# Kernel optimization log

Hardware: AMD Instinct MI355X
Metric: run time of the kernel (lower is better)

Reference implementation:

```python
import jax, jax.numpy as jnp
import numpy as np
import math

B, S, D, NH = 2, 2048, 1024, 16
DK = D // NH
E, TOPK, MOE_H, NSH = 8, 2, 1024, 2
SH_H = MOE_H * NSH
EPS = 1e-6


def setup_inputs() -> dict:
    key = jax.random.key(0)
    ks = jax.random.split(key, 24)
    p = lambda k, shape: jax.random.normal(k, shape, jnp.float32) * 0.02
    x = jax.random.normal(ks[0], (B, S, D), jnp.float32)
    # RoPE tables: freqs_cis = exp(i * t * theta^{-2j/dk}), passed as cos/sin
    inv = 1.0 / (10000.0 ** (np.arange(0, DK, 2, dtype=np.float32) / DK))
    ang = np.outer(np.arange(S, dtype=np.float32), inv)
    freqs_cos = jnp.asarray(np.cos(ang), jnp.float32)
    freqs_sin = jnp.asarray(np.sin(ang), jnp.float32)
    mask = jnp.triu(jnp.full((S, S), -1e9, jnp.float32), k=1)  # causal additive mask
    return {
        'x': x, 'freqs_cos': freqs_cos, 'freqs_sin': freqs_sin, 'mask': mask,
        'wq': p(ks[1], (D, D)), 'wk': p(ks[2], (D, D)),
        'wv': p(ks[3], (D, D)), 'wo': p(ks[4], (D, D)),
        'attn_norm_w': jnp.ones((D,), jnp.float32),
        'ffn_norm_w': jnp.ones((D,), jnp.float32),
        'gate_w': p(ks[5], (E, D)), 'gate_b': p(ks[6], (E,)),
        'w1': p(ks[7], (E, MOE_H, D)), 'b1': p(ks[8], (E, MOE_H)),
        'w2': p(ks[9], (E, D, MOE_H)), 'b2': p(ks[10], (E, D)),
        'w3': p(ks[11], (E, MOE_H, D)), 'b3': p(ks[12], (E, MOE_H)),
        'sg_w': p(ks[13], (SH_H, D)), 'su_w': p(ks[14], (SH_H, D)),
        'sd_w': p(ks[15], (D, SH_H)),
    }


def rmsnorm(x, w):
    f = x.astype(jnp.float32)
    y = f * jax.lax.rsqrt(jnp.mean(f * f, axis=-1, keepdims=True) + EPS)
    return y.astype(x.dtype) * w


def rope(t, cos, sin):
    # t: [b, s, h, dk]; pairs (t[2j], t[2j+1]) as complex, multiplied by e^{i ang}
    tr, ti = t[..., 0::2], t[..., 1::2]
    c, s = cos[None, :, None, :], sin[None, :, None, :]
    outr = tr * c - ti * s
    outi = tr * s + ti * c
    return jnp.stack([outr, outi], axis=-1).reshape(t.shape)


def reference(x, freqs_cos, freqs_sin, mask, wq, wk, wv, wo, attn_norm_w, ffn_norm_w,
              gate_w, gate_b, w1, b1, w2, b2, w3, b3, sg_w, su_w, sd_w):
    b, s, d = x.shape
    # --- attention with RoPE ---
    h = rmsnorm(x, attn_norm_w)
    q = (h @ wq.T).reshape(b, s, NH, DK)
    k = (h @ wk.T).reshape(b, s, NH, DK)
    v = (h @ wv.T).reshape(b, s, NH, DK)
    q = rope(q, freqs_cos, freqs_sin)
    k = rope(k, freqs_cos, freqs_sin)
    scale = 1.0 / math.sqrt(DK)
    q = q.transpose(0, 2, 1, 3)
    k = k.transpose(0, 2, 1, 3)
    v = v.transpose(0, 2, 1, 3)
    scores = jnp.einsum('bhqd,bhkd->bhqk', q, k) * scale + mask
    # NOTE: source divides by sqrt(d_k) a second time before softmax (faithful quirk)
    attn = jax.nn.softmax(scores * scale, axis=-1)
    o = jnp.einsum('bhqk,bhkd->bhqd', attn, v).transpose(0, 2, 1, 3).reshape(b, s, d)
    x = x + o @ wo.T
    # --- MoE FFN ---
    hf = rmsnorm(x, ffn_norm_w).reshape(-1, d)                 # [T, D]
    gscores = jax.nn.softmax(hf @ gate_w.T + gate_b, axis=-1)  # [T, E]
    _, idx = jax.lax.top_k(gscores, TOPK)                      # bias is None -> topk on scores
    weights = jnp.take_along_axis(gscores, idx, axis=1)        # original_scores gather
    wmask = (jax.nn.one_hot(idx, E, dtype=hf.dtype) * weights[..., None]).sum(1)  # [T, E]
    shared = (jax.nn.silu(hf @ sg_w.T) * (hf @ su_w.T)) @ sd_w.T
    a1 = jnp.einsum('td,ehd->teh', hf, w1) + b1
    a3 = jnp.einsum('td,ehd->teh', hf, w3) + b3
    eo = jnp.einsum('teh,edh->ted', jax.nn.silu(a1) * a3, w2) + b2  # [T, E, D]
    router = jnp.einsum('te,ted->td', wmask, eo)
    return x + (shared + router).reshape(x.shape)
```

## Files before the change

### kernel.cpp

```cpp
#include <hip/hip_runtime.h>


typedef unsigned short u16;
typedef __attribute__((ext_vector_type(8))) short bh8;
typedef __attribute__((ext_vector_type(4))) float fv4;
typedef __attribute__((ext_vector_type(4))) unsigned uv4;
typedef __attribute__((ext_vector_type(2))) int iv2;

#define LOG2E 1.4426950408889634f
#define MAX_TILES 71

__device__ __forceinline__ float b2f(u16 u) {
  return __builtin_bit_cast(float, ((unsigned)u) << 16);
}
__device__ __forceinline__ u16 f2b(float f) {
  unsigned x = __builtin_bit_cast(unsigned, f);
  return (u16)((x + 0x7fffu + ((x >> 16) & 1u)) >> 16);
}
__device__ __forceinline__ fv4 mfma16(bh8 a, bh8 b, fv4 c) {
  return __builtin_amdgcn_mfma_f32_16x16x32_bf16(a, b, c, 0, 0, 0);
}
__device__ __forceinline__ unsigned cvtpk(float lo, float hi) {
  unsigned r;
  asm("v_cvt_pk_bf16_f32 %0, %1, %2" : "=v"(r) : "v"(lo), "v"(hi));
  return r;
}

#define GLD16(g, l)                                                        \
  __builtin_amdgcn_global_load_lds(                                        \
      (const __attribute__((address_space(1))) void*)(g),                  \
      (__attribute__((address_space(3))) void*)(l), 16, 0, 0)

__device__ __forceinline__ bh8 lds_frag(const u16* base, int row, int b8) {
  int off = row * 128 + ((b8 * 16) ^ ((row & 7) << 4));
  return *(const bh8*)((const char*)base + off);
}

template <int MODE, int TM = 128>
__global__ __launch_bounds__(256) void gemm_bt(
    const u16* __restrict__ A, const u16* __restrict__ B, int M, int N, int K,
    u16* __restrict__ Cb, float* __restrict__ Cf,
    const float* __restrict__ add1, const float* __restrict__ add2,
    const float* __restrict__ bias, const int* __restrict__ tmeta,
    const int* __restrict__ etok) {
  constexpr int MR = TM / 32;
  __shared__ u16 As[TM * 64];
  __shared__ u16 Bs[128 * 64];
  const int lane = threadIdx.x & 63;
  const int wid = threadIdx.x >> 6;
  const int wr = wid >> 1, wc = wid & 1;
  const int n0 = blockIdx.x * 128;
  const int rr = lane >> 3;
  const int b8s = (lane & 7) ^ rr;
  const int ldA = (MODE == 6) ? M : K;

  int m0 = 0, e = 0, m0l = 0, cnt = 0, row0 = 0;
  const u16* Bp = B;
  if constexpr (MODE == 6 || MODE == 8) {
    int tile = blockIdx.y;
    if (tile >= tmeta[0]) return;
    e = tmeta[16 + tile * 4];
    m0l = tmeta[17 + tile * 4];
    cnt = tmeta[18 + tile * 4];
    row0 = tmeta[19 + tile * 4];
    Bp = B + (size_t)e * N * K;
  } else {
    m0 = blockIdx.y * TM;
  }

  const u16* Arow[MR];
  const u16* Brow[4];
#pragma unroll
  for (int i = 0; i < MR; ++i) {
    int c = wid * MR + i;
    int row = c * 8 + rr;
    if constexpr (MODE == 8) {
      int li = m0l + row;
      li = li < cnt ? li : cnt - 1;
      int tok = etok[e * 4096 + li];
      Arow[i] = A + (size_t)tok * ldA + b8s * 8;
    } else if constexpr (MODE == 6) {
      Arow[i] = A + (size_t)(row0 + row) * ldA + b8s * 8;
    } else {
      Arow[i] = A + (size_t)(m0 + row) * ldA + b8s * 8;
    }
  }
#pragma unroll
  for (int i = 0; i < 4; ++i)
    Brow[i] = Bp + (size_t)(n0 + (wid * 4 + i) * 8 + rr) * K + b8s * 8;

  fv4 acc[MR][4] = {};
  for (int k0 = 0; k0 < K; k0 += 64) {
    __syncthreads();
#pragma unroll
    for (int i = 0; i < MR; ++i)
      GLD16(Arow[i] + k0, &As[(wid * MR + i) * 512]);
#pragma unroll
    for (int i = 0; i < 4; ++i)
      GLD16(Brow[i] + k0, &Bs[(wid * 4 + i) * 512]);
    __syncthreads();
#pragma unroll
    for (int ks = 0; ks < 2; ++ks) {
      int b8 = ks * 4 + (lane >> 4);
      bh8 af[MR], bf[4];
#pragma unroll
      for (int mi = 0; mi < MR; ++mi)
        af[mi] = lds_frag(As, wr * (16 * MR) + mi * 16 + (lane & 15), b8);
#pragma unroll
      for (int ni = 0; ni < 4; ++ni)
        bf[ni] = lds_frag(Bs, wc * 64 + ni * 16 + (lane & 15), b8);
      __builtin_amdgcn_s_setprio(1);
#pragma unroll
      for (int mi = 0; mi < MR; ++mi)
#pragma unroll
        for (int ni = 0; ni < 4; ++ni)
          acc[mi][ni] = mfma16(af[mi], bf[ni], acc[mi][ni]);
      __builtin_amdgcn_s_setprio(0);
    }
  }

  const int rbase = (MODE == 6 || MODE == 8) ? row0 : m0;
  const int r0b = rbase + wr * (16 * MR) + (lane >> 4) * 4;

  if constexpr (MODE == 7 || MODE == 8) {
    const int OUTN = N >> 1;
    const int colb = (n0 >> 1) + wc * 32;
    const float* bb1 = nullptr;
    const float* bb3 = nullptr;
    if constexpr (MODE == 8) {
      bb1 = add1 + (size_t)e * OUTN;
      bb3 = add2 + (size_t)e * OUTN;
    }
#pragma unroll
    for (int mi = 0; mi < MR; ++mi) {
#pragma unroll
      for (int ni = 0; ni < 2; ++ni) {
        int c = colb + ni * 16 + (lane & 15);
#pragma unroll
        for (int r = 0; r < 4; ++r) {
          int row = r0b + mi * 16 + r;
          float xg = acc[mi][ni][r];
          float yu = acc[mi][ni + 2][r];
          if constexpr (MODE == 8) {
            xg += bb1[c];
            yu += bb3[c];
          }
          float s = xg / (1.f + __expf(-xg));
          Cb[(size_t)row * OUTN + c] = f2b(s * yu);
        }
      }
    }
  } else {
    const int c0b = n0 + wc * 64 + (lane & 15);
    const float* bb = nullptr;
    if constexpr (MODE == 6) bb = bias + (size_t)e * N;
#pragma unroll
    for (int mi = 0; mi < MR; ++mi) {
#pragma unroll
      for (int ni = 0; ni < 4; ++ni) {
        int c = c0b + ni * 16;
#pragma unroll
        for (int r = 0; r < 4; ++r) {
          int row = r0b + mi * 16 + r;
          size_t idx = (size_t)row * N + c;
          float v = acc[mi][ni][r];
          if constexpr (MODE == 0) Cb[idx] = f2b(v);
          else if constexpr (MODE == 1) Cf[idx] = add1[idx] + v;
          else if constexpr (MODE == 4) Cf[idx] = add1[idx] + add2[idx] + v;
          else Cb[idx] = f2b(v + bb[c]);
        }
      }
    }
  }
}

__global__ __launch_bounds__(256) void rmsnorm_bf16(
    const float* __restrict__ x, const float* __restrict__ w,
    u16* __restrict__ out) {
  int t = blockIdx.x;
  const float* xr = x + (size_t)t * 1024;
  fv4 v = *(const fv4*)(xr + threadIdx.x * 4);
  float ss = v[0] * v[0] + v[1] * v[1] + v[2] * v[2] + v[3] * v[3];
#pragma unroll
  for (int off = 1; off < 64; off <<= 1) ss += __shfl_xor(ss, off);
  __shared__ float red[4];
  int lane = threadIdx.x & 63, wid = threadIdx.x >> 6;
  if (lane == 0) red[wid] = ss;
  __syncthreads();
  float inv = rsqrtf((red[0] + red[1] + red[2] + red[3]) * (1.0f / 1024.f) + 1e-6f);
  u16* op = out + (size_t)t * 1024 + threadIdx.x * 4;
  const float* wp = w + threadIdx.x * 4;
#pragma unroll
  for (int i = 0; i < 4; ++i) op[i] = f2b(v[i] * inv * wp[i]);
}

__global__ __launch_bounds__(256) void rope_repack(
    const u16* __restrict__ qkv, const float* __restrict__ fc,
    const float* __restrict__ fs, u16* __restrict__ qr, u16* __restrict__ kr,
    u16* __restrict__ vt, int S) {
  __shared__ u16 tile[64][65];
  const int s0 = blockIdx.x * 64;
  const int b = blockIdx.y;
  const int h0 = blockIdx.z * 4;
#pragma unroll 4
  for (int it = 0; it < 32; ++it) {
    int idx = threadIdx.x + it * 256;
    int tl = idx >> 7, rem = idx & 127;
    int h = h0 + (rem >> 5), i = rem & 31;
    int s = s0 + tl;
    float c = fc[s * 32 + i], sn = fs[s * 32 + i];
    size_t src = ((size_t)(b * S + s)) * 3072 + h * 64 + 2 * i;
    size_t dst = ((size_t)((b * 16 + h) * S + s)) * 64 + 2 * i;
    float a0 = b2f(qkv[src]), a1 = b2f(qkv[src + 1]);
    qr[dst] = f2b(a0 * c - a1 * sn);
    qr[dst + 1] = f2b(a0 * sn + a1 * c);
    float b0 = b2f(qkv[src + 1024]), b1 = b2f(qkv[src + 1025]);
    kr[dst] = f2b(b0 * c - b1 * sn);
    kr[dst + 1] = f2b(b0 * sn + b1 * c);
  }
  for (int hh = 0; hh < 4; ++hh) {
    int h = h0 + hh;
    __syncthreads();
    for (int cc = threadIdx.x; cc < 512; cc += 256) {
      int tl = cc >> 3, d8 = cc & 7;
      bh8 val = *(const bh8*)(qkv + ((size_t)(b * S + s0 + tl)) * 3072 + 2048 +
                              h * 64 + d8 * 8);
#pragma unroll
      for (int j = 0; j < 8; ++j) tile[tl][d8 * 8 + j] = (u16)val[j];
    }
    __syncthreads();
    for (int cc = threadIdx.x; cc < 512; cc += 256) {
      int d = cc >> 3, pg = cc & 7;
      int sbase = 16 * (pg >> 2) + 4 * (pg & 3);
      bh8 o;
#pragma unroll
      for (int j = 0; j < 8; ++j)
        o[j] = (short)tile[sbase + (j & 3) + ((j >> 2) << 5)][d];
      *(bh8*)(vt + ((size_t)((b * 16 + h) * 64 + d)) * S + s0 + pg * 8) = o;
    }
  }
}

__global__ __launch_bounds__(256) void attn_fwd(
    const u16* __restrict__ qr, const u16* __restrict__ kr,
    const u16* __restrict__ vt, u16* __restrict__ ob, int S, int NHc) {
  __shared__ u16 Ks[2][64 * 64];
  __shared__ u16 Vs[2][64 * 64];
  const int lane = threadIdx.x & 63;
  const int wid = threadIdx.x >> 6;
  const int g = lane >> 4;
  const int l15 = lane & 15;
  const int bh = blockIdx.x;
  const int ia = blockIdx.y;
  const int nq = S / 64;
  const int qa0 = ia * 64;
  const int qb0 = (nq - 1 - ia) * 64;
  const int b = bh / NHc, h = bh % NHc;
  const u16* qbase = qr + (size_t)bh * S * 64;
  const u16* kb = kr + (size_t)bh * S * 64;
  const u16* vb = vt + (size_t)bh * 64 * S;
  const float SC = 0.015625f * LOG2E;
  const int rr = lane >> 3;
  const int b8s = (lane & 7) ^ rr;

  bh8 ONES;
#pragma unroll
  for (int j = 0; j < 8; ++j) ONES[j] = (short)0x3f80;

  bh8 qfA[2], qfB[2];
  {
    const u16* qp = qbase + (size_t)(qa0 + wid * 16 + l15) * 64 + g * 8;
    qfA[0] = *(const bh8*)qp;
    qfA[1] = *(const bh8*)(qp + 32);
    qp = qbase + (size_t)(qb0 + wid * 16 + l15) * 64 + g * 8;
    qfB[0] = *(const bh8*)qp;
    qfB[1] = *(const bh8*)(qp + 32);
  }
  fv4 oaccA[4] = {}, oaccB[4] = {};
  fv4 lA = {}, lB = {};
  float mA = -1e30f, mB = -1e30f;
  const int nktB = nq - ia;

  auto stage = [&](int buf, int j0) {
#pragma unroll
    for (int i = 0; i < 2; ++i) {
      int c = wid * 2 + i;
      int row = c * 8 + rr;
      GLD16(kb + (size_t)(j0 + row) * 64 + b8s * 8, &Ks[buf][c * 512]);
      GLD16(vb + (size_t)row * S + j0 + b8s * 8, &Vs[buf][c * 512]);
    }
  };
  stage(0, 0);

  auto process = [&](const bh8 (&kf)[2][4], const bh8 (&vf)[2][4], int j0,
                     int q0x, bh8* qf, fv4* oacc, float& mrow, fv4& lrowC) {
    const int q_my = q0x + wid * 16 + l15;
    fv4 st[4] = {};
    __builtin_amdgcn_s_setprio(1);
#pragma unroll
    for (int ks = 0; ks < 2; ++ks)
#pragma unroll
      for (int jt = 0; jt < 4; ++jt)
        st[jt] = mfma16(kf[ks][jt], qf[ks], st[jt]);
    __builtin_amdgcn_s_setprio(0);

    float sr[4][4];
    float mloc = -1e30f;
    const int jb = j0 + 4 * g;
    if (j0 + 63 > q0x + wid * 16) {
#pragma unroll
      for (int jt = 0; jt < 4; ++jt)
#pragma unroll
        for (int r = 0; r < 4; ++r) {
          int j = jb + jt * 16 + r;
          float s = (j <= q_my) ? st[jt][r] : -1e30f;
          sr[jt][r] = s;
          mloc = fmaxf(mloc, s);
        }
    } else {
#pragma unroll
      for (int jt = 0; jt < 4; ++jt)
#pragma unroll
        for (int r = 0; r < 4; ++r) {
          sr[jt][r] = st[jt][r];
          mloc = fmaxf(mloc, st[jt][r]);
        }
    }
    mloc = fmaxf(mloc, __shfl_xor(mloc, 16));
    mloc = fmaxf(mloc, __shfl_xor(mloc, 32));
    mloc *= SC;
    bool defer = __all(mloc <= mrow + 8.f);
    if (!defer) {
      float mnew = fmaxf(mrow, mloc);
      float sfac = exp2f(mrow - mnew);
      mrow = mnew;
      float sfC[4];
#pragma unroll
      for (int r = 0; r < 4; ++r) sfC[r] = __shfl(sfac, g * 4 + r);
#pragma unroll
      for (int dt = 0; dt < 4; ++dt)
#pragma unroll
        for (int r = 0; r < 4; ++r) oacc[dt][r] *= sfC[r];
#pragma unroll
      for (int r = 0; r < 4; ++r) lrowC[r] *= sfC[r];
    }
    float p[4][4];
#pragma unroll
    for (int jt = 0; jt < 4; ++jt)
#pragma unroll
      for (int r = 0; r < 4; ++r)
        p[jt][r] = exp2f(fmaf(sr[jt][r], SC, -mrow));

    __builtin_amdgcn_s_setprio(1);
    fv4 racc = {};
#pragma unroll
    for (int ks = 0; ks < 2; ++ks) {
      uv4 w;
      w[0] = cvtpk(p[ks][0], p[ks][1]);
      w[1] = cvtpk(p[ks][2], p[ks][3]);
      w[2] = cvtpk(p[ks + 2][0], p[ks + 2][1]);
      w[3] = cvtpk(p[ks + 2][2], p[ks + 2][3]);
      bh8 pa = __builtin_bit_cast(bh8, w);
      racc = mfma16(pa, ONES, racc);
#pragma unroll
      for (int dt = 0; dt < 4; ++dt)
        oacc[dt] = mfma16(pa, vf[ks][dt], oacc[dt]);
    }
    __builtin_amdgcn_s_setprio(0);
#pragma unroll
    for (int r = 0; r < 4; ++r) lrowC[r] += racc[r];
  };

  for (int kt = 0; kt < nktB; ++kt) {
    const int j0 = kt * 64;
    __syncthreads();
    if (kt + 1 < nktB) stage((kt + 1) & 1, (kt + 1) * 64);
    const u16* Kc = Ks[kt & 1];
    const u16* Vc = Vs[kt & 1];
    bh8 kf[2][4], vf[2][4];
#pragma unroll
    for (int ks = 0; ks < 2; ++ks) {
      int b8 = ks * 4 + g;
#pragma unroll
      for (int jt = 0; jt < 4; ++jt)
        kf[ks][jt] = lds_frag(Kc, jt * 16 + l15, b8);
#pragma unroll
      for (int dt = 0; dt < 4; ++dt)
        vf[ks][dt] = lds_frag(Vc, dt * 16 + l15, b8);
    }
    process(kf, vf, j0, qb0, qfB, oaccB, mB, lB);
    if (kt <= ia) process(kf, vf, j0, qa0, qfA, oaccA, mA, lA);
  }

  auto wout = [&](fv4* oacc, fv4 lrowC, int q0x) {
#pragma unroll
    for (int dt = 0; dt < 4; ++dt)
#pragma unroll
      for (int r = 0; r < 4; ++r) {
        int row = q0x + wid * 16 + g * 4 + r;
        int col = dt * 16 + l15;
        ob[((size_t)b * S + row) * 1024 + h * 64 + col] =
            f2b(oacc[dt][r] / lrowC[r]);
      }
  };
  wout(oaccA, lA, qa0);
  wout(oaccB, lB, qb0);
}

__global__ __launch_bounds__(256) void gate_topk(
    const float* __restrict__ x2, const float* __restrict__ nw,
    const float* __restrict__ gw, const float* __restrict__ gb,
    int* __restrict__ topk_e, float* __restrict__ topk_w) {
  int t = blockIdx.x * 4 + (threadIdx.x >> 6);
  int lane = threadIdx.x & 63;
  const float* xr = x2 + (size_t)t * 1024;
  float hv[16];
  float ss = 0.f;
#pragma unroll
  for (int i = 0; i < 4; ++i) {
    fv4 v = *(const fv4*)(xr + lane * 16 + i * 4);
#pragma unroll
    for (int j = 0; j < 4; ++j) {
      hv[i * 4 + j] = v[j];
      ss += v[j] * v[j];
    }
  }
#pragma unroll
  for (int off = 1; off < 64; off <<= 1) ss += __shfl_xor(ss, off);
  float inv = rsqrtf(ss * (1.0f / 1024.f) + 1e-6f);
  const fv4* nwp = (const fv4*)(nw + lane * 16);
#pragma unroll
  for (int i = 0; i < 4; ++i) {
    fv4 wv = nwp[i];
#pragma unroll
    for (int j = 0; j < 4; ++j) hv[i * 4 + j] *= inv * wv[j];
  }
  float logit[8];
#pragma unroll
  for (int e = 0; e < 8; ++e) {
    const fv4* wp = (const fv4*)(gw + (size_t)e * 1024 + lane * 16);
    float s = 0.f;
#pragma unroll
    for (int i = 0; i < 4; ++i) {
      fv4 wv = wp[i];
#pragma unroll
      for (int j = 0; j < 4; ++j) s += hv[i * 4 + j] * wv[j];
    }
    logit[e] = s;
  }
#pragma unroll
  for (int off = 1; off < 64; off <<= 1)
#pragma unroll
    for (int e = 0; e < 8; ++e) logit[e] += __shfl_xor(logit[e], off);
  if (lane == 0) {
#pragma unroll
    for (int e = 0; e < 8; ++e) logit[e] += gb[e];
    float mx = logit[0];
#pragma unroll
    for (int e = 1; e < 8; ++e) mx = fmaxf(mx, logit[e]);
    float pe[8], se = 0.f;
#pragma unroll
    for (int e = 0; e < 8; ++e) { pe[e] = __expf(logit[e] - mx); se += pe[e]; }
    float rs = 1.f / se;
#pragma unroll
    for (int e = 0; e < 8; ++e) pe[e] *= rs;
    int i0 = 0;
    float b0 = pe[0];
#pragma unroll
    for (int e = 1; e < 8; ++e)
      if (pe[e] > b0) { b0 = pe[e]; i0 = e; }
    int i1 = -1;
    float b1v = -1.f;
#pragma unroll
    for (int e = 0; e < 8; ++e)
      if (e != i0 && pe[e] > b1v) { b1v = pe[e]; i1 = e; }
    topk_e[2 * t] = i0;
    topk_e[2 * t + 1] = i1;
    topk_w[2 * t] = b0;
    topk_w[2 * t + 1] = b1v;
  }
}

__global__ __launch_bounds__(512) void route_tokens(
    const int* __restrict__ topk_e, int* __restrict__ pos_of,
    int* __restrict__ etok, int* __restrict__ meta, int T2) {
  __shared__ int scnt[8];
  const int e = threadIdx.x >> 6;
  const int lane = threadIdx.x & 63;
  int base = 0;
  for (int i0 = 0; i0 < T2; i0 += 128) {
    iv2 te = *(const iv2*)(topk_e + i0 + lane * 2);
    unsigned long long m0 = __ballot(te[0] == e);
    unsigned long long m1 = __ballot(te[1] == e);
    unsigned long long lt = (1ull << lane) - 1;
    int pre = __popcll(m0 & lt) + __popcll(m1 & lt);
    if (te[0] == e) {
      int pos = base + pre;
      etok[e * 4096 + pos] = (i0 >> 1) + lane;
      pos_of[i0 + lane * 2] = pos;
      ++pre;
    }
    if (te[1] == e) {
      int pos = base + pre;
      etok[e * 4096 + pos] = (i0 >> 1) + lane;
      pos_of[i0 + lane * 2 + 1] = pos;
    }
    base += __popcll(m0) + __popcll(m1);
  }
  if (lane == 0) scnt[e] = base;
  __syncthreads();
  if (threadIdx.x == 0) {
    int tt = 0, rb = 0;
#pragma unroll
    for (int e2 = 0; e2 < 8; ++e2) {
      meta[1 + e2] = rb;
      int c = scnt[e2];
      int nt = (c + 127) >> 7;
      for (int i = 0; i < nt; ++i) {
        meta[16 + tt * 4] = e2;
        meta[17 + tt * 4] = i * 128;
        meta[18 + tt * 4] = c;
        meta[19 + tt * 4] = rb + i * 128;
        ++tt;
      }
      rb += nt * 128;
    }
    meta[0] = tt;
  }
}

__global__ __launch_bounds__(128) void combine_router(
    const u16* __restrict__ eo, const int* __restrict__ topk_e,
    const float* __restrict__ topk_w, const int* __restrict__ pos_of,
    const int* __restrict__ meta, float* __restrict__ router) {
  int t = blockIdx.x;
  int c = threadIdx.x * 8;
  int e0 = topk_e[2 * t], e1 = topk_e[2 * t + 1];
  float w0 = topk_w[2 * t], w1 = topk_w[2 * t + 1];
  int r0 = meta[1 + e0] + pos_of[2 * t];
  int r1 = meta[1 + e1] + pos_of[2 * t + 1];
  bh8 v0 = *(const bh8*)(eo + (size_t)r0 * 1024 + c);
  bh8 v1 = *(const bh8*)(eo + (size_t)r1 * 1024 + c);
  float* rp = router + (size_t)t * 1024 + c;
#pragma unroll
  for (int j = 0; j < 8; ++j)
    rp[j] = w0 * b2f((u16)v0[j]) + w1 * b2f((u16)v1[j]);
}

__global__ __launch_bounds__(256) void f2b_convert(
    const float* __restrict__ src, u16* __restrict__ dst) {
  size_t i = ((size_t)blockIdx.x * 256 + threadIdx.x) * 8;
  fv4 a = *(const fv4*)(src + i);
  fv4 b = *(const fv4*)(src + i + 4);
  bh8 o;
#pragma unroll
  for (int j = 0; j < 4; ++j) o[j] = (short)f2b(a[j]);
#pragma unroll
  for (int j = 0; j < 4; ++j) o[4 + j] = (short)f2b(b[j]);
  *(bh8*)(dst + i) = o;
}

__global__ __launch_bounds__(256) void f2b_convert_ilv(
    const float* __restrict__ src, u16* __restrict__ dst, int half,
    int seg_shift) {
  size_t i = ((size_t)blockIdx.x * 256 + threadIdx.x) * 8;
  int r = (int)(i >> 10), col = (int)(i & 1023);
  int rl = r & ((1 << seg_shift) - 1), e = r >> seg_shift;
  int dstrow = (e << (seg_shift + 1)) + ((rl >> 5) << 6) + (rl & 31) +
               (half << 5);
  fv4 a = *(const fv4*)(src + i);
  fv4 b = *(const fv4*)(src + i + 4);
  bh8 o;
#pragma unroll
  for (int j = 0; j < 4; ++j) o[j] = (short)f2b(a[j]);
#pragma unroll
  for (int j = 0; j < 4; ++j) o[4 + j] = (short)f2b(b[j]);
  *(bh8*)(dst + (size_t)dstrow * 1024 + col) = o;
}

extern "C" void kernel_launch(void* const* d_in, const int* in_sizes, int n_in,
                              void* d_out, int out_size, void* d_ws,
                              size_t ws_size, hipStream_t stream) {
  (void)in_sizes; (void)n_in; (void)out_size; (void)ws_size;
  const int Sc = 2048, Dc = 1024, NHc = 16, Tc = 4096, SH = 2048;

  const float* x   = (const float*)d_in[0];
  const float* fc  = (const float*)d_in[1];
  const float* fs  = (const float*)d_in[2];
  const float* wq  = (const float*)d_in[4];
  const float* wk  = (const float*)d_in[5];
  const float* wv  = (const float*)d_in[6];
  const float* wo  = (const float*)d_in[7];
  const float* anw = (const float*)d_in[8];
  const float* fnw = (const float*)d_in[9];
  const float* gw  = (const float*)d_in[10];
  const float* gb  = (const float*)d_in[11];
  const float* w1  = (const float*)d_in[12];
  const float* b1  = (const float*)d_in[13];
  const float* w2  = (const float*)d_in[14];
  const float* b2  = (const float*)d_in[15];
  const float* w3  = (const float*)d_in[16];
  const float* b3  = (const float*)d_in[17];
  const float* sgw = (const float*)d_in[18];
  const float* suw = (const float*)d_in[19];
  const float* sdw = (const float*)d_in[20];
  float* out = (float*)d_out;

  char* base = (char*)d_ws;
  size_t off = 0;
  auto alloc = [&](size_t bytes) -> void* {
    void* p = base + off;
    off += (bytes + 255) & ~(size_t)255;
    return p;
  };
  u16* wqkv_b = (u16*)alloc(2ull * 3072 * 1024);
  u16* wo_b   = (u16*)alloc(2ull * 1024 * 1024);
  u16* sgu_b  = (u16*)alloc(2ull * 4096 * 1024);
  u16* sdw_b  = (u16*)alloc(2ull * 1024 * 2048);
  u16* w13_b  = (u16*)alloc(2ull * 8 * 2048 * 1024);
  u16* w2_b   = (u16*)alloc(2ull * 8 * 1024 * 1024);
  char* regA = (char*)alloc(2ull * Tc * 4096);
  char* regB = (char*)alloc(2ull * (size_t)MAX_TILES * 128 * 2048);
  float* x2  = (float*)alloc(4ull * Tc * Dc);
  u16* hs_b  = (u16*)alloc(2ull * Tc * SH);
  int* topk_e = (int*)alloc(2ull * Tc * 4);
  float* topk_w = (float*)alloc(2ull * Tc * 4);
  int* pos_of = (int*)alloc(2ull * Tc * 4);
  int* etok = (int*)alloc(8ull * 4096 * 4);
  int* meta = (int*)alloc(512 * 4);

  u16* qkv_out = (u16*)regA;
  u16* eo_c    = (u16*)regA;
  u16* h_b  = (u16*)regB;
  u16* qr   = (u16*)regB;
  u16* kr   = (u16*)(regB + 2ull * Tc * Dc);
  u16* vt_  = (u16*)(regB + 4ull * Tc * Dc);
  u16* o_b  = (u16*)(regB + 6ull * Tc * Dc);
  u16* a13_c = (u16*)regB;
  float* router = (float*)regB;
  u16* hf_b = wqkv_b;

  auto conv = [&](const float* s, u16* d, size_t n) {
    f2b_convert<<<dim3((unsigned)(n / 2048)), 256, 0, stream>>>(s, d);
  };
  conv(wq, wqkv_b, (size_t)Dc * Dc);
  conv(wk, wqkv_b + 1048576, (size_t)Dc * Dc);
  conv(wv, wqkv_b + 2097152, (size_t)Dc * Dc);
  conv(wo, wo_b, (size_t)Dc * Dc);
  conv(sdw, sdw_b, (size_t)Dc * SH);
  conv(w2, w2_b, 8ull * 1024 * 1024);
  f2b_convert_ilv<<<1024, 256, 0, stream>>>(sgw, sgu_b, 0, 11);
  f2b_convert_ilv<<<1024, 256, 0, stream>>>(suw, sgu_b, 1, 11);
  f2b_convert_ilv<<<4096, 256, 0, stream>>>(w1, w13_b, 0, 10);
  f2b_convert_ilv<<<4096, 256, 0, stream>>>(w3, w13_b, 1, 10);

  rmsnorm_bf16<<<Tc, 256, 0, stream>>>(x, anw, h_b);
  gemm_bt<0><<<dim3(3072 / 128, Tc / 128), 256, 0, stream>>>(
      h_b, wqkv_b, Tc, 3072, Dc, qkv_out, nullptr, nullptr, nullptr, nullptr,
      nullptr, nullptr);
  rope_repack<<<dim3(Sc / 64, 2, 4), 256, 0, stream>>>(qkv_out, fc, fs, qr, kr,
                                                       vt_, Sc);
  attn_fwd<<<dim3(2 * NHc, Sc / 128), 256, 0, stream>>>(qr, kr, vt_, o_b, Sc,
                                                        NHc);
  gemm_bt<1, 64><<<dim3(Dc / 128, Tc / 64), 256, 0, stream>>>(
      o_b, wo_b, Tc, Dc, Dc, nullptr, x2, x, nullptr, nullptr, nullptr,
      nullptr);

  rmsnorm_bf16<<<Tc, 256, 0, stream>>>(x2, fnw, hf_b);
  gate_topk<<<Tc / 4, 256, 0, stream>>>(x2, fnw, gw, gb, topk_e, topk_w);
  route_tokens<<<1, 512, 0, stream>>>(topk_e, pos_of, etok, meta, 2 * Tc);

  gemm_bt<7><<<dim3(4096 / 128, Tc / 128), 256, 0, stream>>>(
      hf_b, sgu_b, Tc, 4096, Dc, hs_b, nullptr, nullptr, nullptr, nullptr,
      nullptr, nullptr);

  gemm_bt<8><<<dim3(2048 / 128, MAX_TILES), 256, 0, stream>>>(
      hf_b, w13_b, Tc, 2048, Dc, a13_c, nullptr, b1, b3, nullptr, meta, etok);
  gemm_bt<6><<<dim3(Dc / 128, MAX_TILES), 256, 0, stream>>>(
      a13_c, w2_b, 1024, Dc, 1024, eo_c, nullptr, nullptr, nullptr,
      b2, meta, etok);
  combine_router<<<Tc, 128, 0, stream>>>(eo_c, topk_e, topk_w, pos_of, meta,
                                         router);

  gemm_bt<4, 64><<<dim3(Dc / 128, Tc / 64), 256, 0, stream>>>(
      hs_b, sdw_b, Tc, Dc, SH, nullptr, out, x2, router, nullptr, nullptr,
      nullptr);
}
```

Before: 426.2 us.

## Fuse router combine into down-proj epilogue, fold ffn rmsnorm into gate, swizzle XCDs

Removes the combine_router kernel by having the shared down-projection GEMM epilogue gather the two expert outputs through precomputed row ids and add them weighted. The ffn rmsnorm kernel is dropped because gate_topk now writes the normalized bf16 activations itself. route_tokens computes a per-slot row id table. All GEMMs remap block indices so consecutive tiles land on the same XCD for L2 locality. The intent is to save launches and the fp32 router round trip through memory, at the cost of scattered bf16 gathers in the epilogue and a heavier gate kernel.

Measured after the change: 414.9 us. 2.7% less time.

```diff
diff --git a/kernel.cpp b/kernel.cpp
--- a/kernel.cpp
+++ b/kernel.cpp
@@ -24,6 +24,17 @@
   unsigned r;
   asm("v_cvt_pk_bf16_f32 %0, %1, %2" : "=v"(r) : "v"(lo), "v"(hi));
   return r;
+}
+
+__device__ __forceinline__ void xcd_swizzle(int& bx, int& by) {
+  int gx = gridDim.x;
+  int nwg = gx * gridDim.y;
+  int flat = by * gx + bx;
+  int q = nwg >> 3, r = nwg & 7;
+  int xcd = flat & 7, idx = flat >> 3;
+  int swz = (xcd < r ? xcd * (q + 1) : r * (q + 1) + (xcd - r) * q) + idx;
+  by = swz / gx;
+  bx = swz - by * gx;
 }
 
 #define GLD16(g, l)                                                        \
@@ -46,10 +57,12 @@
   constexpr int MR = TM / 32;
   __shared__ u16 As[TM * 64];
   __shared__ u16 Bs[128 * 64];
+  int bx = blockIdx.x, by = blockIdx.y;
+  xcd_swizzle(bx, by);
   const int lane = threadIdx.x & 63;
   const int wid = threadIdx.x >> 6;
   const int wr = wid >> 1, wc = wid & 1;
-  const int n0 = blockIdx.x * 128;
+  const int n0 = bx * 128;
   const int rr = lane >> 3;
   const int b8s = (lane & 7) ^ rr;
   const int ldA = (MODE == 6) ? M : K;
@@ -57,7 +70,7 @@
   int m0 = 0, e = 0, m0l = 0, cnt = 0, row0 = 0;
   const u16* Bp = B;
   if constexpr (MODE == 6 || MODE == 8) {
-    int tile = blockIdx.y;
+    int tile = by;
     if (tile >= tmeta[0]) return;
     e = tmeta[16 + tile * 4];
     m0l = tmeta[17 + tile * 4];
@@ -65,7 +78,7 @@
     row0 = tmeta[19 + tile * 4];
     Bp = B + (size_t)e * N * K;
   } else {
-    m0 = blockIdx.y * TM;
+    m0 = by * TM;
   }
 
   const u16* Arow[MR];
@@ -121,6 +134,7 @@
 
   const int rbase = (MODE == 6 || MODE == 8) ? row0 : m0;
   const int r0b = rbase + wr * (16 * MR) + (lane >> 4) * 4;
+  const int c0b = n0 + wc * 64 + (lane & 15);
 
   if constexpr (MODE == 7 || MODE == 8) {
     const int OUTN = N >> 1;
@@ -150,8 +164,26 @@
         }
       }
     }
+  } else if constexpr (MODE == 9) {
+#pragma unroll
+    for (int mi = 0; mi < MR; ++mi) {
+#pragma unroll
+      for (int r = 0; r < 4; ++r) {
+        int row = r0b + mi * 16 + r;
+        int g0 = tmeta[2 * row], g1 = tmeta[2 * row + 1];
+        float w0 = bias[2 * row], w1 = bias[2 * row + 1];
+        const u16* e0p = Cb + (size_t)g0 * 1024;
+        const u16* e1p = Cb + (size_t)g1 * 1024;
+#pragma unroll
+        for (int ni = 0; ni < 4; ++ni) {
+          int c = c0b + ni * 16;
+          size_t idx = (size_t)row * N + c;
+          Cf[idx] = add1[idx] + acc[mi][ni][r] + w0 * b2f(e0p[c]) +
+                    w1 * b2f(e1p[c]);
+        }
+      }
+    }
   } else {
-    const int c0b = n0 + wc * 64 + (lane & 15);
     const float* bb = nullptr;
     if constexpr (MODE == 6) bb = bias + (size_t)e * N;
 #pragma unroll
@@ -166,7 +198,6 @@
           float v = acc[mi][ni][r];
           if constexpr (MODE == 0) Cb[idx] = f2b(v);
           else if constexpr (MODE == 1) Cf[idx] = add1[idx] + v;
-          else if constexpr (MODE == 4) Cf[idx] = add1[idx] + add2[idx] + v;
           else Cb[idx] = f2b(v + bb[c]);
         }
       }
@@ -410,7 +441,8 @@
 __global__ __launch_bounds__(256) void gate_topk(
     const float* __restrict__ x2, const float* __restrict__ nw,
     const float* __restrict__ gw, const float* __restrict__ gb,
-    int* __restrict__ topk_e, float* __restrict__ topk_w) {
+    int* __restrict__ topk_e, float* __restrict__ topk_w,
+    u16* __restrict__ hf) {
   int t = blockIdx.x * 4 + (threadIdx.x >> 6);
   int lane = threadIdx.x & 63;
   const float* xr = x2 + (size_t)t * 1024;
@@ -434,6 +466,17 @@
     fv4 wv = nwp[i];
 #pragma unroll
     for (int j = 0; j < 4; ++j) hv[i * 4 + j] *= inv * wv[j];
+  }
+  {
+    bh8 o0, o1;
+#pragma unroll
+    for (int j = 0; j < 8; ++j) {
+      o0[j] = (short)f2b(hv[j]);
+      o1[j] = (short)f2b(hv[8 + j]);
+    }
+    u16* hp = hf + (size_t)t * 1024 + lane * 16;
+    *(bh8*)hp = o0;
+    *(bh8*)(hp + 8) = o1;
   }
   float logit[8];
 #pragma unroll
@@ -483,8 +526,9 @@
 
 __global__ __launch_bounds__(512) void route_tokens(
     const int* __restrict__ topk_e, int* __restrict__ pos_of,
-    int* __restrict__ etok, int* __restrict__ meta, int T2) {
-  __shared__ int scnt[8];
+    int* __restrict__ etok, int* __restrict__ meta, int* __restrict__ rowid,
+    int T2) {
+  __shared__ int scnt[8], sbase[8];
   const int e = threadIdx.x >> 6;
   const int lane = threadIdx.x & 63;
   int base = 0;
@@ -513,7 +557,7 @@
     int tt = 0, rb = 0;
 #pragma unroll
     for (int e2 = 0; e2 < 8; ++e2) {
-      meta[1 + e2] = rb;
+      sbase[e2] = rb;
       int c = scnt[e2];
       int nt = (c + 127) >> 7;
       for (int i = 0; i < nt; ++i) {
@@ -527,24 +571,9 @@
     }
     meta[0] = tt;
   }
-}
-
-__global__ __launch_bounds__(128) void combine_router(
-    const u16* __restrict__ eo, const int* __restrict__ topk_e,
-    const float* __restrict__ topk_w, const int* __restrict__ pos_of,
-    const int* __restrict__ meta, float* __restrict__ router) {
-  int t = blockIdx.x;
-  int c = threadIdx.x * 8;
-  int e0 = topk_e[2 * t], e1 = topk_e[2 * t + 1];
-  float w0 = topk_w[2 * t], w1 = topk_w[2 * t + 1];
-  int r0 = meta[1 + e0] + pos_of[2 * t];
-  int r1 = meta[1 + e1] + pos_of[2 * t + 1];
-  bh8 v0 = *(const bh8*)(eo + (size_t)r0 * 1024 + c);
-  bh8 v1 = *(const bh8*)(eo + (size_t)r1 * 1024 + c);
-  float* rp = router + (size_t)t * 1024 + c;
-#pragma unroll
-  for (int j = 0; j < 8; ++j)
-    rp[j] = w0 * b2f((u16)v0[j]) + w1 * b2f((u16)v1[j]);
+  __syncthreads();
+  for (int i = threadIdx.x; i < T2; i += 512)
+    rowid[i] = sbase[topk_e[i]] + pos_of[i];
 }
 
 __global__ __launch_bounds__(256) void f2b_convert(
@@ -626,6 +655,7 @@
   int* topk_e = (int*)alloc(2ull * Tc * 4);
   float* topk_w = (float*)alloc(2ull * Tc * 4);
   int* pos_of = (int*)alloc(2ull * Tc * 4);
+  int* rowid = (int*)alloc(2ull * Tc * 4);
   int* etok = (int*)alloc(8ull * 4096 * 4);
   int* meta = (int*)alloc(512 * 4);
 
@@ -637,7 +667,6 @@
   u16* vt_  = (u16*)(regB + 4ull * Tc * Dc);
   u16* o_b  = (u16*)(regB + 6ull * Tc * Dc);
   u16* a13_c = (u16*)regB;
-  float* router = (float*)regB;
   u16* hf_b = wqkv_b;
 
   auto conv = [&](const float* s, u16* d, size_t n) {
@@ -666,9 +695,10 @@
       o_b, wo_b, Tc, Dc, Dc, nullptr, x2, x, nullptr, nullptr, nullptr,
       nullptr);
 
-  rmsnorm_bf16<<<Tc, 256, 0, stream>>>(x2, fnw, hf_b);
-  gate_topk<<<Tc / 4, 256, 0, stream>>>(x2, fnw, gw, gb, topk_e, topk_w);
-  route_tokens<<<1, 512, 0, stream>>>(topk_e, pos_of, etok, meta, 2 * Tc);
+  gate_topk<<<Tc / 4, 256, 0, stream>>>(x2, fnw, gw, gb, topk_e, topk_w,
+                                        hf_b);
+  route_tokens<<<1, 512, 0, stream>>>(topk_e, pos_of, etok, meta, rowid,
+                                      2 * Tc);
 
   gemm_bt<7><<<dim3(4096 / 128, Tc / 128), 256, 0, stream>>>(
       hf_b, sgu_b, Tc, 4096, Dc, hs_b, nullptr, nullptr, nullptr, nullptr,
@@ -679,10 +709,8 @@
   gemm_bt<6><<<dim3(Dc / 128, MAX_TILES), 256, 0, stream>>>(
       a13_c, w2_b, 1024, Dc, 1024, eo_c, nullptr, nullptr, nullptr,
       b2, meta, etok);
-  combine_router<<<Tc, 128, 0, stream>>>(eo_c, topk_e, topk_w, pos_of, meta,
-                                         router);
-
-  gemm_bt<4, 64><<<dim3(Dc / 128, Tc / 64), 256, 0, stream>>>(
-      hs_b, sdw_b, Tc, Dc, SH, nullptr, out, x2, router, nullptr, nullptr,
+
+  gemm_bt<9, 64><<<dim3(Dc / 128, Tc / 64), 256, 0, stream>>>(
+      hs_b, sdw_b, Tc, Dc, SH, eo_c, out, x2, nullptr, topk_w, rowid,
       nullptr);
 }
```
